# Performance work log

Hardware: AMD Instinct MI355X
Metric: run time of the kernel (lower is better)

The kernel has to match this reference:

```python
import jax, jax.numpy as jnp
import numpy as np
from jax import lax

K = 512   # codebook size (clusternumber)
D = 16    # feature dim = channels after conv4 (arch=2)

def conv2d_same(x, w, b):
    # x: (B,C,H,W), w: (O,I,3,3) -> same-padded stride-1 conv
    y = lax.conv_general_dilated(x, w, (1, 1), 'SAME',
                                 dimension_numbers=('NCHW', 'OIHW', 'NCHW'))
    return y + b[None, :, None, None]

def maxpool2(x):
    return lax.reduce_window(x, -jnp.inf, lax.max, (1, 1, 2, 2), (1, 1, 2, 2), 'VALID')

def setup_inputs() -> dict:
    key = jax.random.key(0)
    ks = jax.random.split(key, 16)
    s = 0.05
    return {
        'x':        jax.random.normal(ks[0], (64, 3, 64, 64), jnp.float32),
        'w1':       jax.random.normal(ks[1], (16, 3, 3, 3), jnp.float32) * s,
        'b1':       jnp.zeros((16,), jnp.float32),
        'w2':       jax.random.normal(ks[2], (16, 16, 3, 3), jnp.float32) * s,
        'b2':       jnp.zeros((16,), jnp.float32),
        'w3':       jax.random.normal(ks[3], (24, 16, 3, 3), jnp.float32) * s,
        'b3':       jnp.zeros((24,), jnp.float32),
        'w4':       jax.random.normal(ks[4], (16, 24, 3, 3), jnp.float32) * s,
        'b4':       jnp.zeros((16,), jnp.float32),
        'codebook': jax.random.normal(ks[5], (K, D), jnp.float32) * 0.1,
        'sigma':    jax.random.uniform(ks[6], (K,), jnp.float32, 0.05, 0.15),
        'l1_w':     jax.random.normal(ks[7], (20, K), jnp.float32) * (1.0 / np.sqrt(K)),
        'l1_b':     jnp.zeros((20,), jnp.float32),
        'l2_w':     jax.random.normal(ks[8], (10, 20), jnp.float32) * (1.0 / np.sqrt(20)),
        'l2_b':     jnp.zeros((10,), jnp.float32),
    }

def reference(x, w1, b1, w2, b2, w3, b3, w4, b4, codebook, sigma,
              l1_w, l1_b, l2_w, l2_b):
    # CNN trunk (arch=2, bofnumber=4): conv,conv,pool,conv,conv with relu
    h = jax.nn.relu(conv2d_same(x, w1, b1))
    h = jax.nn.relu(conv2d_same(h, w2, b2))
    h = maxpool2(h)
    h = jax.nn.relu(conv2d_same(h, w3, b3))
    h = jax.nn.relu(conv2d_same(h, w4, b4))
    B, C, H, W = h.shape
    f = h.reshape(B, C, H * W).transpose(0, 2, 1)          # (B, N, D)
    # squared euclidean distance via norm expansion (same math as
    # sum(|x - c|^2), avoids materializing (B,K,N,D))
    f2 = jnp.sum(f * f, axis=2)                            # (B, N)
    c2 = jnp.sum(codebook * codebook, axis=1)              # (K,)
    cross = jnp.einsum('bnd,kd->bkn', f, codebook)         # (B, K, N)
    dist = f2[:, None, :] + c2[None, :, None] - 2.0 * cross
    a = jnp.exp(-dist * sigma[None, :, None])              # RBF membership
    # F.normalize(p=1, dim=1) over the K codebook axis
    a = a / jnp.clip(jnp.sum(jnp.abs(a), axis=1, keepdims=True), 1e-12)
    pooled = jnp.mean(a, axis=2)                           # (B, K)
    z = jax.nn.relu(pooled @ l1_w.T + l1_b)
    return z @ l2_w.T + l2_b                               # (B, 10)
```

## Files before the change

kernel.cpp:

```cpp
#include <hip/hip_runtime.h>
#include <hip/hip_bf16.h>

#define KCB 512
#define DF  16
#define BATCH 64

__device__ __forceinline__ float bperm(int addr, float v) {
    return __int_as_float(__builtin_amdgcn_ds_bpermute(addr, __float_as_int(v)));
}

__global__ __launch_bounds__(256) void wtrans_kernel(
    const float* __restrict__ w1, const float* __restrict__ w2,
    const float* __restrict__ w3, const float* __restrict__ w4,
    float* __restrict__ wt1, float* __restrict__ wt2,
    float* __restrict__ wt3, float* __restrict__ wt4)
{
    int i = blockIdx.x * 256 + threadIdx.x;
    if (i < 432) {
        int o = i & 15, rest = i >> 4;
        int kx = rest % 3, ky = (rest / 3) % 3, c = rest / 9;
        wt1[i] = w1[((o * 3 + c) * 3 + ky) * 3 + kx];
        return;
    }
    i -= 432;
    if (i < 2304) {
        int o = i & 15, rest = i >> 4;
        int kx = rest % 3, ky = (rest / 3) % 3, c = rest / 9;
        wt2[i] = w2[((o * 16 + c) * 3 + ky) * 3 + kx];
        return;
    }
    i -= 2304;
    if (i < 3456) {
        int o = i % 24, rest = i / 24;
        int kx = rest % 3, ky = (rest / 3) % 3, c = rest / 9;
        wt3[i] = w3[((o * 16 + c) * 3 + ky) * 3 + kx];
        return;
    }
    i -= 3456;
    if (i < 3456) {
        int o = i & 15, rest = i >> 4;
        int kx = rest % 3, ky = (rest / 3) % 3, c = rest / 9;
        wt4[i] = w4[((o * 24 + c) * 3 + ky) * 3 + kx];
    }
}

template<int CIN, int COUT_T, int COUT_TOTAL>
__global__ __launch_bounds__(256) void conv_row64_kernel(
    const float* __restrict__ in, const float* __restrict__ wt,
    const float* __restrict__ bias, float* __restrict__ out)
{
    const int H = 64, W = 64;
    const int lane = threadIdx.x & 63;
    const int wv = threadIdx.x >> 6;
    const int y = blockIdx.x * 4 + wv;
    const int og = blockIdx.y * COUT_T;
    const int b = blockIdx.z;
    const int x = lane;
    const int xl = max(x - 1, 0);
    const int xr = min(x + 1, W - 1);

    float acc[COUT_T];
#pragma unroll
    for (int o = 0; o < COUT_T; ++o) acc[o] = bias[og + o];

#pragma unroll
    for (int c = 0; c < CIN; ++c) {
        const float* ip = in + ((size_t)(b * CIN + c) * H) * W;
#pragma unroll
        for (int ky = 0; ky < 3; ++ky) {
            int ry = y + ky - 1;
            int ryc = min(max(ry, 0), H - 1);
            const float* rp = ip + ryc * W;
            float tc = rp[x], tl = rp[xl], tr = rp[xr];
            bool ok = (ry == ryc);
            float vc = ok ? tc : 0.f;
            float vl = (ok && x > 0)     ? tl : 0.f;
            float vr = (ok && x < W - 1) ? tr : 0.f;
            const float* wp = wt + ((c * 3 + ky) * 3) * COUT_TOTAL + og;
#pragma unroll
            for (int o = 0; o < COUT_T; ++o) acc[o] = fmaf(vl, wp[o], acc[o]);
#pragma unroll
            for (int o = 0; o < COUT_T; ++o) acc[o] = fmaf(vc, wp[COUT_TOTAL + o], acc[o]);
#pragma unroll
            for (int o = 0; o < COUT_T; ++o) acc[o] = fmaf(vr, wp[2 * COUT_TOTAL + o], acc[o]);
        }
    }
#pragma unroll
    for (int o = 0; o < COUT_T; ++o)
        out[((b * COUT_TOTAL + og + o) * H + y) * W + x] = fmaxf(acc[o], 0.f);
}

__global__ __launch_bounds__(256) void conv2_pool_kernel(
    const float* __restrict__ in, const float* __restrict__ wt,
    const float* __restrict__ bias, float* __restrict__ out)
{
    const int CIN = 16, COUT_T = 8, H = 64, W = 64;
    const int lane = threadIdx.x & 63;
    const int wv = threadIdx.x >> 6;
    const int r = blockIdx.x * 4 + wv;
    const int y0 = r * 2;
    const int og = blockIdx.y * COUT_T;
    const int b = blockIdx.z;
    const int x = lane;
    const int xl = max(x - 1, 0);
    const int xr = min(x + 1, W - 1);
    const int aR = ((lane + 1) & 63) << 2;

    float acc0[COUT_T], acc1[COUT_T];
#pragma unroll
    for (int o = 0; o < COUT_T; ++o) { acc0[o] = bias[og + o]; acc1[o] = bias[og + o]; }

#pragma unroll 4
    for (int c = 0; c < CIN; ++c) {
        const float* ip = in + ((size_t)(b * CIN + c) * H) * W;
        float v[4], vl[4], vr[4];
#pragma unroll
        for (int j = 0; j < 4; ++j) {
            int ry = y0 - 1 + j;
            int ryc = min(max(ry, 0), H - 1);
            const float* rp = ip + ryc * W;
            float tc = rp[x], tl = rp[xl], tr = rp[xr];
            bool ok = (ry == ryc);
            v[j]  = ok ? tc : 0.f;
            vl[j] = (ok && x > 0)     ? tl : 0.f;
            vr[j] = (ok && x < W - 1) ? tr : 0.f;
        }
#pragma unroll
        for (int ky = 0; ky < 3; ++ky) {
            const float* wp = wt + ((c * 3 + ky) * 3) * 16 + og;
#pragma unroll
            for (int kx = 0; kx < 3; ++kx) {
                float a0 = (kx == 0) ? vl[ky]     : (kx == 1) ? v[ky]     : vr[ky];
                float a1 = (kx == 0) ? vl[ky + 1] : (kx == 1) ? v[ky + 1] : vr[ky + 1];
                const float* wq = wp + kx * 16;
#pragma unroll
                for (int o = 0; o < COUT_T; ++o) {
                    float w = wq[o];
                    acc0[o] = fmaf(a0, w, acc0[o]);
                    acc1[o] = fmaf(a1, w, acc1[o]);
                }
            }
        }
    }

    const int px = x >> 1;
#pragma unroll
    for (int o = 0; o < COUT_T; ++o) {
        float m = fmaxf(fmaxf(acc0[o], acc1[o]), 0.f);
        m = fmaxf(m, bperm(aR, m));
        if ((x & 1) == 0)
            out[((b * 16 + og + o) * 32 + r) * 32 + px] = m;
    }
}

template<int CIN, int COUT_T, int COUT_TOTAL>
__global__ __launch_bounds__(256) void conv_rp32_kernel(
    const float* __restrict__ in, const float* __restrict__ wt,
    const float* __restrict__ bias, float* __restrict__ out)
{
    const int H = 32, W = 32;
    const int lane = threadIdx.x & 63;
    const int wv = threadIdx.x >> 6;
    const int p = blockIdx.x * 4 + wv;
    const int og = blockIdx.y * COUT_T;
    const int b = blockIdx.z;
    const int h = lane >> 5;
    const int x = lane & 31;
    const int y = p * 2 + h;
    const int xl = max(x - 1, 0);
    const int xr = min(x + 1, W - 1);

    float acc[COUT_T];
#pragma unroll
    for (int o = 0; o < COUT_T; ++o) acc[o] = bias[og + o];

#pragma unroll 4
    for (int c = 0; c < CIN; ++c) {
        const float* ip = in + ((size_t)(b * CIN + c) * H) * W;
        float v[3], vl[3], vr[3];
#pragma unroll
        for (int d = 0; d < 3; ++d) {
            int ry = y + d - 1;
            int ryc = min(max(ry, 0), H - 1);
            const float* rp = ip + ryc * W;
            float tc = rp[x], tl = rp[xl], tr = rp[xr];
            bool ok = (ry == ryc);
            v[d]  = ok ? tc : 0.f;
            vl[d] = (ok && x > 0)     ? tl : 0.f;
            vr[d] = (ok && x < W - 1) ? tr : 0.f;
        }
#pragma unroll
        for (int ky = 0; ky < 3; ++ky) {
#pragma unroll
            for (int kx = 0; kx < 3; ++kx) {
                float a = (kx == 0) ? vl[ky] : (kx == 1) ? v[ky] : vr[ky];
                const float* wq = wt + ((c * 3 + ky) * 3 + kx) * COUT_TOTAL + og;
#pragma unroll
                for (int o = 0; o < COUT_T; ++o)
                    acc[o] = fmaf(a, wq[o], acc[o]);
            }
        }
    }
#pragma unroll
    for (int o = 0; o < COUT_T; ++o)
        out[((b * COUT_TOTAL + og + o) * H + y) * W + x] = fmaxf(acc[o], 0.f);
}

__global__ __launch_bounds__(256) void conv4_ft_kernel(
    const float* __restrict__ in, const float* __restrict__ wt,
    const float* __restrict__ bias, float* __restrict__ ft,
    float* __restrict__ f2p)
{
    const int CIN = 24, COUT_T = 4, H = 32, W = 32;
    const int lane = threadIdx.x & 63;
    const int wv = threadIdx.x >> 6;
    const int p = blockIdx.x * 4 + wv;
    const int g = blockIdx.y;
    const int og = g * COUT_T;
    const int b = blockIdx.z;
    const int h = lane >> 5;
    const int x = lane & 31;
    const int y = p * 2 + h;
    const int xl = max(x - 1, 0);
    const int xr = min(x + 1, W - 1);

    float acc[COUT_T];
#pragma unroll
    for (int o = 0; o < COUT_T; ++o) acc[o] = bias[og + o];

#pragma unroll 4
    for (int c = 0; c < CIN; ++c) {
        const float* ip = in + ((size_t)(b * CIN + c) * H) * W;
        float v[3], vl[3], vr[3];
#pragma unroll
        for (int d = 0; d < 3; ++d) {
            int ry = y + d - 1;
            int ryc = min(max(ry, 0), H - 1);
            const float* rp = ip + ryc * W;
            float tc = rp[x], tl = rp[xl], tr = rp[xr];
            bool ok = (ry == ryc);
            v[d]  = ok ? tc : 0.f;
            vl[d] = (ok && x > 0)     ? tl : 0.f;
            vr[d] = (ok && x < W - 1) ? tr : 0.f;
        }
#pragma unroll
        for (int ky = 0; ky < 3; ++ky) {
#pragma unroll
            for (int kx = 0; kx < 3; ++kx) {
                float a = (kx == 0) ? vl[ky] : (kx == 1) ? v[ky] : vr[ky];
                const float* wq = wt + ((c * 3 + ky) * 3 + kx) * 16 + og;
#pragma unroll
                for (int o = 0; o < COUT_T; ++o)
                    acc[o] = fmaf(a, wq[o], acc[o]);
            }
        }
    }

    const size_t pix = (size_t)b * 1024 + y * W + x;
    float v0 = fmaxf(acc[0], 0.f), v1 = fmaxf(acc[1], 0.f);
    float v2 = fmaxf(acc[2], 0.f), v3 = fmaxf(acc[3], 0.f);
    *(float4*)(ft + pix * 16 + og) = make_float4(v0, v1, v2, v3);
    float s2 = v0 * v0;
    s2 = fmaf(v1, v1, s2);
    s2 = fmaf(v2, v2, s2);
    s2 = fmaf(v3, v3, s2);
    f2p[(size_t)g * (BATCH * 1024) + pix] = s2;
}

__global__ __launch_bounds__(512) void bof_kernel(
    const float* __restrict__ ft, const float* __restrict__ f2p,
    const float* __restrict__ codebook, const float* __restrict__ sigma,
    float* __restrict__ partial)
{
    const int J = 16;
    const int PIX = 64;
    const int b = blockIdx.y;
    const int chunk = blockIdx.x;
    const int t = threadIdx.x;
    const int lane = t & 63;
    const int w = t >> 6;

    __shared__ float s_e[KCB][J + 1];
    __shared__ float s_q[8][16];
    __shared__ float s_dinv[J];
    __shared__ float s_tmp[4][PIX];
    __shared__ float s_f2[PIX];

    const size_t base = (size_t)b * 1024 + chunk * PIX;
    if (t < 256) {
        const int g = t >> 6, j = t & 63;
        s_tmp[g][j] = f2p[(size_t)g * (BATCH * 1024) + base + j];
    }

    float cb[DF];
    {
        const float4* cq = (const float4*)(codebook + (size_t)t * DF);
        float4 a0 = cq[0], a1 = cq[1], a2 = cq[2], a3 = cq[3];
        cb[0]=a0.x; cb[1]=a0.y; cb[2]=a0.z; cb[3]=a0.w;
        cb[4]=a1.x; cb[5]=a1.y; cb[6]=a1.z; cb[7]=a1.w;
        cb[8]=a2.x; cb[9]=a2.y; cb[10]=a2.z; cb[11]=a2.w;
        cb[12]=a3.x; cb[13]=a3.y; cb[14]=a3.z; cb[15]=a3.w;
    }
    float c2 = 0.f;
#pragma unroll
    for (int d = 0; d < DF; ++d) c2 = fmaf(cb[d], cb[d], c2);
    const float sg = sigma[t];

    __syncthreads();
    if (t < PIX) s_f2[t] = (s_tmp[0][t] + s_tmp[1][t]) + (s_tmp[2][t] + s_tmp[3][t]);
    __syncthreads();

    float acc = 0.f;

    for (int jb = 0; jb < PIX / J; ++jb) {
        const int j0 = jb * J;
        float e[J];
#pragma unroll
        for (int jj = 0; jj < J; ++jj) {
            const float* fp = ft + (base + j0 + jj) * DF;
            float dot = 0.f;
#pragma unroll
            for (int d = 0; d < DF; ++d) dot = fmaf(fp[d], cb[d], dot);
            float f2c = s_f2[j0 + jj] + c2;
            float dist = fmaf(-2.f, dot, f2c);
            e[jj] = __expf(-dist * sg);
            s_e[t][jj] = e[jj];
        }
        __syncthreads();

        {
            const int c   = t & 15;
            const int seg = t >> 4;
            float ps = 0.f;
#pragma unroll
            for (int r = 0; r < 16; ++r) ps += s_e[seg * 16 + r][c];
            ps += __shfl_xor(ps, 16);
            ps += __shfl_xor(ps, 32);
            if (lane < 16) s_q[w][lane] = ps;
        }
        __syncthreads();

        if (t < J) {
            float dsum = 0.f;
#pragma unroll
            for (int i = 0; i < 8; ++i) dsum += s_q[i][t];
            s_dinv[t] = 1.f / fmaxf(dsum, 1e-12f);
        }
        __syncthreads();

#pragma unroll
        for (int jj = 0; jj < J; ++jj)
            acc = fmaf(e[jj], s_dinv[jj], acc);
    }
    partial[((size_t)b * 16 + chunk) * KCB + t] = acc;
}

__global__ __launch_bounds__(512) void tail_kernel(
    const float* __restrict__ partial,
    const float* __restrict__ l1w, const float* __restrict__ l1b,
    const float* __restrict__ l2w, const float* __restrict__ l2b,
    float* __restrict__ out)
{
    const int b = blockIdx.x;
    const int t = threadIdx.x;
    __shared__ float s_pool[KCB];
    __shared__ float s_z[20];

    float s = 0.f;
#pragma unroll
    for (int c = 0; c < 16; ++c)
        s += partial[((size_t)b * 16 + c) * KCB + t];
    s_pool[t] = s * (1.0f / 1024.0f);
    __syncthreads();

    if (t < 320) {
        const int row = t >> 4;
        const int l   = t & 15;
        float a = 0.f;
        const float* wr = l1w + (size_t)row * KCB;
#pragma unroll
        for (int m = 0; m < 32; ++m)
            a = fmaf(s_pool[l + 16 * m], wr[l + 16 * m], a);
#pragma unroll
        for (int off = 1; off < 16; off <<= 1)
            a += __shfl_xor(a, off);
        if (l == 0) s_z[row] = fmaxf(a + l1b[row], 0.f);
    }
    __syncthreads();

    if (t < 10) {
        float s2 = l2b[t];
#pragma unroll
        for (int j = 0; j < 20; ++j) s2 = fmaf(s_z[j], l2w[t * 20 + j], s2);
        out[b * 10 + t] = s2;
    }
}

extern "C" void kernel_launch(void* const* d_in, const int* in_sizes, int n_in,
                              void* d_out, int out_size, void* d_ws, size_t ws_size,
                              hipStream_t stream)
{
    const float* x        = (const float*)d_in[0];
    const float* w1       = (const float*)d_in[1];
    const float* b1       = (const float*)d_in[2];
    const float* w2       = (const float*)d_in[3];
    const float* b2       = (const float*)d_in[4];
    const float* w3       = (const float*)d_in[5];
    const float* b3       = (const float*)d_in[6];
    const float* w4       = (const float*)d_in[7];
    const float* b4       = (const float*)d_in[8];
    const float* codebook = (const float*)d_in[9];
    const float* sigma    = (const float*)d_in[10];
    const float* l1w      = (const float*)d_in[11];
    const float* l1b      = (const float*)d_in[12];
    const float* l2w      = (const float*)d_in[13];
    const float* l2b      = (const float*)d_in[14];
    float* out = (float*)d_out;

    float* ws = (float*)d_ws;
    const size_t N_WT1 = 432;
    const size_t N_WT2 = 2304;
    const size_t N_WT3 = 3456;
    const size_t N_WT4 = 3456;
    const size_t N_C1 = (size_t)BATCH * 16 * 64 * 64;
    const size_t N_P  = (size_t)BATCH * 16 * 32 * 32;
    const size_t N_C3 = (size_t)BATCH * 24 * 32 * 32;
    const size_t N_FT = (size_t)BATCH * 1024 * 16;
    const size_t N_F2 = (size_t)4 * BATCH * 1024;
    const size_t N_PART = (size_t)BATCH * 16 * KCB;

    float* wt1  = ws;  ws += N_WT1;
    float* wt2  = ws;  ws += N_WT2;
    float* wt3  = ws;  ws += N_WT3;
    float* wt4  = ws;  ws += N_WT4;
    float* c1   = ws;  ws += N_C1;
    float* p    = ws;  ws += N_P;
    float* c3   = ws;  ws += N_C3;
    float* ft   = ws;  ws += N_FT;
    float* f2p  = ws;  ws += N_F2;
    float* part = ws;  ws += N_PART;

    wtrans_kernel<<<38, 256, 0, stream>>>(w1, w2, w3, w4, wt1, wt2, wt3, wt4);
    conv_row64_kernel<3, 8, 16><<<dim3(16, 2, BATCH), 256, 0, stream>>>(x, wt1, b1, c1);
    conv2_pool_kernel<<<dim3(8, 2, BATCH), 256, 0, stream>>>(c1, wt2, b2, p);
    conv_rp32_kernel<16, 3, 24><<<dim3(4, 8, BATCH), 256, 0, stream>>>(p, wt3, b3, c3);
    conv4_ft_kernel<<<dim3(4, 4, BATCH), 256, 0, stream>>>(c3, wt4, b4, ft, f2p);
    bof_kernel<<<dim3(16, BATCH), 512, 0, stream>>>(ft, f2p, codebook, sigma, part);
    tail_kernel<<<BATCH, 512, 0, stream>>>(part, l1w, l1b, l2w, l2b, out);
}
```

Before: 116.9 us.

## Split conv output channels finer, add occupancy hints, software-pipeline BoF exponent blocks

Halves the output-channel tile in conv2_pool and conv4_ft and doubles their grid y-dimension, so each block does less work and more blocks run. f2p partial sums grow from 4 to 8 groups to match. All conv kernels and the BoF kernel get a min-blocks launch-bounds hint of 8 to force fewer registers. The BoF kernel now computes the next 16-pixel exponent block while the current block's normalization reduction is in flight, using a double-buffered register array and removing one barrier per iteration. The risks are register spills from the occupancy hint, the extra e[2][J] buffer under a 512-thread launch bound, and redundant input reads caused by the finer channel split.

```diff
diff --git a/kernel.cpp b/kernel.cpp
--- a/kernel.cpp
+++ b/kernel.cpp
@@ -45,7 +45,7 @@
 }
 
 template<int CIN, int COUT_T, int COUT_TOTAL>
-__global__ __launch_bounds__(256) void conv_row64_kernel(
+__global__ __launch_bounds__(256, 8) void conv_row64_kernel(
     const float* __restrict__ in, const float* __restrict__ wt,
     const float* __restrict__ bias, float* __restrict__ out)
 {
@@ -90,11 +90,11 @@
         out[((b * COUT_TOTAL + og + o) * H + y) * W + x] = fmaxf(acc[o], 0.f);
 }
 
-__global__ __launch_bounds__(256) void conv2_pool_kernel(
+__global__ __launch_bounds__(256, 8) void conv2_pool_kernel(
     const float* __restrict__ in, const float* __restrict__ wt,
     const float* __restrict__ bias, float* __restrict__ out)
 {
-    const int CIN = 16, COUT_T = 8, H = 64, W = 64;
+    const int CIN = 16, COUT_T = 4, H = 64, W = 64;
     const int lane = threadIdx.x & 63;
     const int wv = threadIdx.x >> 6;
     const int r = blockIdx.x * 4 + wv;
@@ -154,7 +154,7 @@
 }
 
 template<int CIN, int COUT_T, int COUT_TOTAL>
-__global__ __launch_bounds__(256) void conv_rp32_kernel(
+__global__ __launch_bounds__(256, 8) void conv_rp32_kernel(
     const float* __restrict__ in, const float* __restrict__ wt,
     const float* __restrict__ bias, float* __restrict__ out)
 {
@@ -206,12 +206,12 @@
         out[((b * COUT_TOTAL + og + o) * H + y) * W + x] = fmaxf(acc[o], 0.f);
 }
 
-__global__ __launch_bounds__(256) void conv4_ft_kernel(
+__global__ __launch_bounds__(256, 8) void conv4_ft_kernel(
     const float* __restrict__ in, const float* __restrict__ wt,
     const float* __restrict__ bias, float* __restrict__ ft,
     float* __restrict__ f2p)
 {
-    const int CIN = 24, COUT_T = 4, H = 32, W = 32;
+    const int CIN = 24, COUT_T = 2, H = 32, W = 32;
     const int lane = threadIdx.x & 63;
     const int wv = threadIdx.x >> 6;
     const int p = blockIdx.x * 4 + wv;
@@ -258,16 +258,11 @@
 
     const size_t pix = (size_t)b * 1024 + y * W + x;
     float v0 = fmaxf(acc[0], 0.f), v1 = fmaxf(acc[1], 0.f);
-    float v2 = fmaxf(acc[2], 0.f), v3 = fmaxf(acc[3], 0.f);
-    *(float4*)(ft + pix * 16 + og) = make_float4(v0, v1, v2, v3);
-    float s2 = v0 * v0;
-    s2 = fmaf(v1, v1, s2);
-    s2 = fmaf(v2, v2, s2);
-    s2 = fmaf(v3, v3, s2);
-    f2p[(size_t)g * (BATCH * 1024) + pix] = s2;
-}
-
-__global__ __launch_bounds__(512) void bof_kernel(
+    *(float2*)(ft + pix * 16 + og) = make_float2(v0, v1);
+    f2p[(size_t)g * (BATCH * 1024) + pix] = fmaf(v1, v1, v0 * v0);
+}
+
+__global__ __launch_bounds__(512, 8) void bof_kernel(
     const float* __restrict__ ft, const float* __restrict__ f2p,
     const float* __restrict__ codebook, const float* __restrict__ sigma,
     float* __restrict__ partial)
@@ -283,11 +278,11 @@
     __shared__ float s_e[KCB][J + 1];
     __shared__ float s_q[8][16];
     __shared__ float s_dinv[J];
-    __shared__ float s_tmp[4][PIX];
+    __shared__ float s_tmp[8][PIX];
     __shared__ float s_f2[PIX];
 
     const size_t base = (size_t)b * 1024 + chunk * PIX;
-    if (t < 256) {
+    {
         const int g = t >> 6, j = t & 63;
         s_tmp[g][j] = f2p[(size_t)g * (BATCH * 1024) + base + j];
     }
@@ -307,50 +302,65 @@
     const float sg = sigma[t];
 
     __syncthreads();
-    if (t < PIX) s_f2[t] = (s_tmp[0][t] + s_tmp[1][t]) + (s_tmp[2][t] + s_tmp[3][t]);
+    if (t < PIX) {
+        float s = 0.f;
+#pragma unroll
+        for (int g = 0; g < 8; ++g) s += s_tmp[g][t];
+        s_f2[t] = s;
+    }
     __syncthreads();
 
+    float e[2][J];
+#pragma unroll
+    for (int jj = 0; jj < J; ++jj) {
+        const float* fp = ft + (base + jj) * DF;
+        float dot = 0.f;
+#pragma unroll
+        for (int d = 0; d < DF; ++d) dot = fmaf(fp[d], cb[d], dot);
+        float dist = fmaf(-2.f, dot, s_f2[jj] + c2);
+        e[0][jj] = __expf(-dist * sg);
+        s_e[t][jj] = e[0][jj];
+    }
+    __syncthreads();
+
     float acc = 0.f;
-
-    for (int jb = 0; jb < PIX / J; ++jb) {
-        const int j0 = jb * J;
-        float e[J];
-#pragma unroll
-        for (int jj = 0; jj < J; ++jj) {
-            const float* fp = ft + (base + j0 + jj) * DF;
-            float dot = 0.f;
-#pragma unroll
-            for (int d = 0; d < DF; ++d) dot = fmaf(fp[d], cb[d], dot);
-            float f2c = s_f2[j0 + jj] + c2;
-            float dist = fmaf(-2.f, dot, f2c);
-            e[jj] = __expf(-dist * sg);
-            s_e[t][jj] = e[jj];
-        }
-        __syncthreads();
-
+#pragma unroll
+    for (int i = 0; i < 4; ++i) {
+        const int cur = i & 1, nxt = cur ^ 1;
         {
             const int c   = t & 15;
             const int seg = t >> 4;
             float ps = 0.f;
 #pragma unroll
-            for (int r = 0; r < 16; ++r) ps += s_e[seg * 16 + r][c];
+            for (int rr = 0; rr < 16; ++rr) ps += s_e[seg * 16 + rr][c];
             ps += __shfl_xor(ps, 16);
             ps += __shfl_xor(ps, 32);
             if (lane < 16) s_q[w][lane] = ps;
         }
         __syncthreads();
-
         if (t < J) {
             float dsum = 0.f;
 #pragma unroll
-            for (int i = 0; i < 8; ++i) dsum += s_q[i][t];
+            for (int q = 0; q < 8; ++q) dsum += s_q[q][t];
             s_dinv[t] = 1.f / fmaxf(dsum, 1e-12f);
         }
+        if (i < 3) {
+            const int j0 = (i + 1) * J;
+#pragma unroll
+            for (int jj = 0; jj < J; ++jj) {
+                const float* fp = ft + (base + j0 + jj) * DF;
+                float dot = 0.f;
+#pragma unroll
+                for (int d = 0; d < DF; ++d) dot = fmaf(fp[d], cb[d], dot);
+                float dist = fmaf(-2.f, dot, s_f2[j0 + jj] + c2);
+                e[nxt][jj] = __expf(-dist * sg);
+                s_e[t][jj] = e[nxt][jj];
+            }
+        }
         __syncthreads();
-
 #pragma unroll
         for (int jj = 0; jj < J; ++jj)
-            acc = fmaf(e[jj], s_dinv[jj], acc);
+            acc = fmaf(e[cur][jj], s_dinv[jj], acc);
     }
     partial[((size_t)b * 16 + chunk) * KCB + t] = acc;
 }
@@ -426,7 +436,7 @@
     const size_t N_P  = (size_t)BATCH * 16 * 32 * 32;
     const size_t N_C3 = (size_t)BATCH * 24 * 32 * 32;
     const size_t N_FT = (size_t)BATCH * 1024 * 16;
-    const size_t N_F2 = (size_t)4 * BATCH * 1024;
+    const size_t N_F2 = (size_t)8 * BATCH * 1024;
     const size_t N_PART = (size_t)BATCH * 16 * KCB;
 
     float* wt1  = ws;  ws += N_WT1;
@@ -442,9 +452,9 @@
 
     wtrans_kernel<<<38, 256, 0, stream>>>(w1, w2, w3, w4, wt1, wt2, wt3, wt4);
     conv_row64_kernel<3, 8, 16><<<dim3(16, 2, BATCH), 256, 0, stream>>>(x, wt1, b1, c1);
-    conv2_pool_kernel<<<dim3(8, 2, BATCH), 256, 0, stream>>>(c1, wt2, b2, p);
+    conv2_pool_kernel<<<dim3(8, 4, BATCH), 256, 0, stream>>>(c1, wt2, b2, p);
     conv_rp32_kernel<16, 3, 24><<<dim3(4, 8, BATCH), 256, 0, stream>>>(p, wt3, b3, c3);
-    conv4_ft_kernel<<<dim3(4, 4, BATCH), 256, 0, stream>>>(c3, wt4, b4, ft, f2p);
+    conv4_ft_kernel<<<dim3(4, 8, BATCH), 256, 0, stream>>>(c3, wt4, b4, ft, f2p);
     bof_kernel<<<dim3(16, BATCH), 512, 0, stream>>>(ft, f2p, codebook, sigma, part);
     tail_kernel<<<BATCH, 512, 0, stream>>>(part, l1w, l1b, l2w, l2b, out);
 }
```

Result: slower. 222.8 us (+90.6%).
